# Optimization experiments

Measured on AMD Instinct MI355X. Metric: run time of the kernel, lower is better.

## Reference

```python
import jax, jax.numpy as jnp
import numpy as np

B, S, D, H = 4, 2048, 1024, 16
HD = D // H  # head dim = 64


def setup_inputs() -> dict:
    key = jax.random.key(0)
    ks = jax.random.split(key, 5)
    scale = 0.02
    return {
        "x": jax.random.normal(ks[0], (B, S, D), dtype=jnp.float32),
        "w_qkv": jax.random.normal(ks[1], (D, 3 * D), dtype=jnp.float32) * scale,
        "b_qkv": jax.random.normal(ks[2], (3 * D,), dtype=jnp.float32) * scale,
        "w_proj": jax.random.normal(ks[3], (D, D), dtype=jnp.float32) * scale,
        "b_proj": jax.random.normal(ks[4], (D,), dtype=jnp.float32) * scale,
    }


def reference(x, w_qkv, b_qkv, w_proj, b_proj):
    # Fused QKV projection: [B,S,D] @ [D,3D] -> [B,S,3D]
    qkv = jnp.einsum('bsd,de->bse', x, w_qkv) + b_qkv
    q, k, v = jnp.split(qkv, 3, axis=-1)
    # [B,S,D] -> [B,H,S,hd]
    def heads(t):
        return t.reshape(B, S, H, HD).transpose(0, 2, 1, 3)
    q, k, v = heads(q), heads(k), heads(v)
    # Scaled dot-product attention (non-causal, matching torch SDPA defaults)
    scores = jnp.einsum('bhsd,bhtd->bhst', q, k) / jnp.sqrt(jnp.float32(HD))
    attn = jax.nn.softmax(scores, axis=-1)
    out = jnp.einsum('bhst,bhtd->bhsd', attn, v)
    # [B,H,S,hd] -> [B,S,D]
    out = out.transpose(0, 2, 1, 3).reshape(B, S, D)
    return jnp.einsum('bsd,de->bse', out, w_proj) + b_proj
```

## Files before the change

kernel.cpp:

```cpp
#include <hip/hip_runtime.h>
#include <hip/hip_bf16.h>
#include <cstdint>

typedef __attribute__((ext_vector_type(8))) __bf16 bf16x8;
typedef __attribute__((ext_vector_type(4))) __bf16 bf16x4;
typedef __attribute__((ext_vector_type(4))) float f32x4;

#define MFMA16(a, b, c) __builtin_amdgcn_mfma_f32_16x16x32_bf16(a, b, c, 0, 0, 0)

static constexpr float SCQ = 0.18033688f;

__device__ __forceinline__ void gload16(const void* g, void* l) {
  __builtin_amdgcn_global_load_lds(
      (const __attribute__((address_space(1))) void*)g,
      (__attribute__((address_space(3))) void*)l, 16, 0, 0);
}

__global__ __launch_bounds__(256) void conv_x(const float* __restrict__ in,
                                              __bf16* __restrict__ out) {
  const size_t i = ((size_t)blockIdx.x * 256 + threadIdx.x) * 8;
  const float4 v0 = *(const float4*)(in + i);
  const float4 v1 = *(const float4*)(in + i + 4);
  bf16x8 o = {(__bf16)v0.x, (__bf16)v0.y, (__bf16)v0.z, (__bf16)v0.w,
              (__bf16)v1.x, (__bf16)v1.y, (__bf16)v1.z, (__bf16)v1.w};
  *(bf16x8*)(out + i) = o;
}

__global__ __launch_bounds__(256) void conv_wt(const float* __restrict__ W,
                                               __bf16* __restrict__ Wt,
                                               int K, int N) {
  __shared__ float tile[64][65];
  const int nb = blockIdx.x * 64, kb = blockIdx.y * 64;
  const int t = threadIdx.x, tr = t >> 4, tc = t & 15;
  #pragma unroll
  for (int p = 0; p < 4; ++p) {
    const float4 v =
        *(const float4*)(W + (size_t)(kb + p * 16 + tr) * N + nb + tc * 4);
    tile[p * 16 + tr][tc * 4 + 0] = v.x;
    tile[p * 16 + tr][tc * 4 + 1] = v.y;
    tile[p * 16 + tr][tc * 4 + 2] = v.z;
    tile[p * 16 + tr][tc * 4 + 3] = v.w;
  }
  __syncthreads();
  #pragma unroll
  for (int p = 0; p < 4; ++p) {
    const int n = p * 16 + tr, kk = tc * 4;
    bf16x4 o = {(__bf16)tile[kk + 0][n], (__bf16)tile[kk + 1][n],
                (__bf16)tile[kk + 2][n], (__bf16)tile[kk + 3][n]};
    *(bf16x4*)(Wt + (size_t)(nb + n) * K + kb + kk) = o;
  }
}

__global__ __launch_bounds__(256) void qkv_gemm_b(
    const __bf16* __restrict__ A, const __bf16* __restrict__ Bt,
    const float* __restrict__ bias,
    __bf16* __restrict__ Qb, __bf16* __restrict__ Kb, __bf16* __restrict__ Vt)
{
  __shared__ alignas(16) __bf16 a_sh[128 * 32];
  __shared__ alignas(16) __bf16 b_sh[128 * 32];
  const int id = blockIdx.x;
  const int wg = (id & 7) * 192 + (id >> 3);
  const int n0 = (wg % 24) * 128, m0 = (wg / 24) * 128;
  const int t = threadIdx.x, wave = t >> 6, lane = t & 63;
  const int r = lane & 15, g = lane >> 4;
  const int wm = (wave >> 1) * 64, wn = (wave & 1) * 64;
  f32x4 acc[4][4] = {};

  const int srow = wave * 16 + (lane >> 2);
  const int scol = (lane & 3) * 8;
  const __bf16* gA = A + (size_t)(m0 + srow) * 1024 + scol;
  const __bf16* gB = Bt + (size_t)(n0 + srow) * 1024 + scol;
  __bf16* lA = a_sh + wave * 512;
  __bf16* lB = b_sh + wave * 512;

  for (int k0 = 0; k0 < 1024; k0 += 32) {
    __syncthreads();
    gload16(gA + k0, lA);
    gload16(gA + 64 * 1024 + k0, lA + 2048);
    gload16(gB + k0, lB);
    gload16(gB + 64 * 1024 + k0, lB + 2048);
    __syncthreads();
    bf16x8 af[4], bfr[4];
    #pragma unroll
    for (int i = 0; i < 4; ++i)
      af[i] = *(bf16x8*)&a_sh[(wm + i * 16 + r) * 32 + g * 8];
    #pragma unroll
    for (int j = 0; j < 4; ++j)
      bfr[j] = *(bf16x8*)&b_sh[(wn + j * 16 + r) * 32 + g * 8];
    #pragma unroll
    for (int i = 0; i < 4; ++i)
      #pragma unroll
      for (int j = 0; j < 4; ++j)
        acc[i][j] = MFMA16(af[i], bfr[j], acc[i][j]);
  }

  const int which = n0 >> 10;
  const int bb = m0 >> 11;
  const int sbase = (m0 & 2047) + wm;
  #pragma unroll
  for (int j = 0; j < 4; ++j) {
    const int nc = n0 + wn + j * 16 + r;
    const float bv = bias[nc];
    const int hh = (nc & 1023) >> 6;
    const int d = nc & 63;
    #pragma unroll
    for (int i = 0; i < 4; ++i) {
      const int ss0 = sbase + i * 16 + g * 4;
      if (which == 0) {
        #pragma unroll
        for (int rr = 0; rr < 4; ++rr)
          Qb[((size_t)(bb * 16 + hh) * 2048 + ss0 + rr) * 64 + d] =
              (__bf16)((acc[i][j][rr] + bv) * SCQ);
      } else if (which == 1) {
        #pragma unroll
        for (int rr = 0; rr < 4; ++rr)
          Kb[((size_t)(bb * 16 + hh) * 2048 + ss0 + rr) * 64 + d] =
              (__bf16)(acc[i][j][rr] + bv);
      } else {
        bf16x4 vv;
        #pragma unroll
        for (int rr = 0; rr < 4; ++rr) vv[rr] = (__bf16)(acc[i][j][rr] + bv);
        const int v5 = ss0 & 31;
        const int pcol = (ss0 & ~31) + 8 * ((v5 >> 2) & 3) + 4 * (v5 >> 4);
        *(bf16x4*)&Vt[((size_t)(bb * 16 + hh) * 64 + d) * 2048 + pcol] = vv;
      }
    }
  }
}

__global__ __launch_bounds__(256) void proj_gemm_b(
    const __bf16* __restrict__ A, const __bf16* __restrict__ Bt,
    const float* __restrict__ bias, float* __restrict__ out)
{
  __shared__ alignas(16) __bf16 a_sh[128 * 32];
  __shared__ alignas(16) __bf16 b_sh[128 * 32];
  const int id = blockIdx.x;
  const int wg = (id & 7) * 64 + (id >> 3);
  const int n0 = (wg & 7) * 128, m0 = (wg >> 3) * 128;
  const int t = threadIdx.x, wave = t >> 6, lane = t & 63;
  const int r = lane & 15, g = lane >> 4;
  const int wm = (wave >> 1) * 64, wn = (wave & 1) * 64;
  f32x4 acc[4][4] = {};

  const int srow = wave * 16 + (lane >> 2);
  const int scol = (lane & 3) * 8;
  const __bf16* gA = A + (size_t)(m0 + srow) * 1024 + scol;
  const __bf16* gB = Bt + (size_t)(n0 + srow) * 1024 + scol;
  __bf16* lA = a_sh + wave * 512;
  __bf16* lB = b_sh + wave * 512;

  for (int k0 = 0; k0 < 1024; k0 += 32) {
    __syncthreads();
    gload16(gA + k0, lA);
    gload16(gA + 64 * 1024 + k0, lA + 2048);
    gload16(gB + k0, lB);
    gload16(gB + 64 * 1024 + k0, lB + 2048);
    __syncthreads();
    bf16x8 af[4], bfr[4];
    #pragma unroll
    for (int i = 0; i < 4; ++i)
      af[i] = *(bf16x8*)&a_sh[(wm + i * 16 + r) * 32 + g * 8];
    #pragma unroll
    for (int j = 0; j < 4; ++j)
      bfr[j] = *(bf16x8*)&b_sh[(wn + j * 16 + r) * 32 + g * 8];
    #pragma unroll
    for (int i = 0; i < 4; ++i)
      #pragma unroll
      for (int j = 0; j < 4; ++j)
        acc[i][j] = MFMA16(af[i], bfr[j], acc[i][j]);
  }

  #pragma unroll
  for (int j = 0; j < 4; ++j) {
    const int nc = n0 + wn + j * 16 + r;
    const float bv = bias[nc];
    #pragma unroll
    for (int i = 0; i < 4; ++i)
      #pragma unroll
      for (int rr = 0; rr < 4; ++rr)
        out[(size_t)(m0 + wm + i * 16 + g * 4 + rr) * 1024 + nc] =
            acc[i][j][rr] + bv;
  }
}

__global__ __launch_bounds__(256, 4) void attn_kernel(
    const __bf16* __restrict__ Q, const __bf16* __restrict__ K,
    const __bf16* __restrict__ Vt, __bf16* __restrict__ AO)
{
  __shared__ alignas(16) __bf16 k_sh[64][72];
  __shared__ alignas(16) __bf16 v_sh[64][72];

  const int p = blockIdx.x;
  const int hd = (p & 7) + 8 * (p >> 7);
  const int qt = (p >> 3) & 15;
  const int b = hd >> 4, h = hd & 15;

  const int t = threadIdx.x, wave = t >> 6, lane = t & 63;
  const int r = lane & 15, g = lane >> 4;

  const __bf16* Qp = Q + (size_t)hd * (2048 * 64);
  const __bf16* Kp = K + (size_t)hd * (2048 * 64);
  const __bf16* Vp = Vt + (size_t)hd * (64 * 2048);
  const int q0 = qt * 128 + wave * 32;

  const int sr = t >> 2;
  const int sc = (t & 3) * 8;
  const __bf16* gK = Kp + (size_t)sr * 64 + sc;
  const __bf16* gV = Vp + (size_t)sr * 2048 + sc;

  bf16x8 qf[2][2];
  #pragma unroll
  for (int qh = 0; qh < 2; ++qh)
    #pragma unroll
    for (int hh = 0; hh < 2; ++hh)
      qf[qh][hh] =
          *(const bf16x8*)(Qp + (size_t)(q0 + qh * 16 + r) * 64 + hh * 32 + g * 8);

  float mrun[2] = {0.f, 0.f};
  float lrun[2] = {0.f, 0.f};
  f32x4 o[4][2] = {};

  bf16x8 rk0, rk1, rv0, rv1;
  #define LOADT(kk)                                                \
    {                                                              \
      rk0 = *(const bf16x8*)(gK + (size_t)(kk) * 64);              \
      rk1 = *(const bf16x8*)(gK + (size_t)(kk) * 64 + 32);         \
      rv0 = *(const bf16x8*)(gV + (kk));                           \
      rv1 = *(const bf16x8*)(gV + (kk) + 32);                      \
    }

  LOADT(0);

  for (int t32 = 0; t32 < 32; ++t32) {
    __syncthreads();
    *(bf16x8*)&k_sh[sr][sc] = rk0;
    *(bf16x8*)&k_sh[sr][sc + 32] = rk1;
    *(bf16x8*)&v_sh[sr][sc] = rv0;
    *(bf16x8*)&v_sh[sr][sc + 32] = rv1;
    __syncthreads();
    if (t32 < 31) LOADT((t32 + 1) * 64);

    f32x4 sacc[4][2];
    const f32x4 seed0 = {-mrun[0], -mrun[0], -mrun[0], -mrun[0]};
    const f32x4 seed1 = {-mrun[1], -mrun[1], -mrun[1], -mrun[1]};
    __builtin_amdgcn_s_setprio(1);
    #pragma unroll
    for (int kt = 0; kt < 4; ++kt) {
      const bf16x8 kf0 = *(const bf16x8*)&k_sh[kt * 16 + r][g * 8];
      const bf16x8 kf1 = *(const bf16x8*)&k_sh[kt * 16 + r][32 + g * 8];
      f32x4 s0 = MFMA16(kf0, qf[0][0], seed0);
      s0 = MFMA16(kf1, qf[0][1], s0);
      sacc[kt][0] = s0;
      f32x4 s1 = MFMA16(kf0, qf[1][0], seed1);
      s1 = MFMA16(kf1, qf[1][1], s1);
      sacc[kt][1] = s1;
    }
    __builtin_amdgcn_s_setprio(0);

    bf16x8 pf[2][2];
    #pragma unroll
    for (int qh = 0; qh < 2; ++qh) {
      float a0 = fmaxf(fmaxf(sacc[0][qh][0], sacc[0][qh][1]),
                       fmaxf(sacc[0][qh][2], sacc[0][qh][3]));
      float a1 = fmaxf(fmaxf(sacc[1][qh][0], sacc[1][qh][1]),
                       fmaxf(sacc[1][qh][2], sacc[1][qh][3]));
      float a2 = fmaxf(fmaxf(sacc[2][qh][0], sacc[2][qh][1]),
                       fmaxf(sacc[2][qh][2], sacc[2][qh][3]));
      float a3 = fmaxf(fmaxf(sacc[3][qh][0], sacc[3][qh][1]),
                       fmaxf(sacc[3][qh][2], sacc[3][qh][3]));
      const float tm = fmaxf(fmaxf(a0, a1), fmaxf(a2, a3));

      float s = 0.f;
      if (__any(tm > 6.0f)) {
        float rm = fmaxf(tm, __shfl_xor(tm, 16));
        rm = fmaxf(rm, __shfl_xor(rm, 32));
        const float dl = fmaxf(rm, 0.f);
        const float al = exp2f(-dl);
        mrun[qh] += dl;
        #pragma unroll
        for (int kt = 0; kt < 4; ++kt)
          #pragma unroll
          for (int rr = 0; rr < 4; ++rr) {
            const float e = exp2f(sacc[kt][qh][rr] - dl);
            s += e;
            pf[qh][kt >> 1][(kt & 1) * 4 + rr] = (__bf16)e;
          }
        lrun[qh] = lrun[qh] * al + s;
        #pragma unroll
        for (int dt = 0; dt < 4; ++dt)
          #pragma unroll
          for (int rr = 0; rr < 4; ++rr)
            o[dt][qh][rr] *= al;
      } else {
        #pragma unroll
        for (int kt = 0; kt < 4; ++kt)
          #pragma unroll
          for (int rr = 0; rr < 4; ++rr) {
            const float e = exp2f(sacc[kt][qh][rr]);
            s += e;
            pf[qh][kt >> 1][(kt & 1) * 4 + rr] = (__bf16)e;
          }
        lrun[qh] += s;
      }
    }

    __builtin_amdgcn_s_setprio(1);
    #pragma unroll
    for (int c = 0; c < 2; ++c)
      #pragma unroll
      for (int dt = 0; dt < 4; ++dt) {
        const bf16x8 vf = *(const bf16x8*)&v_sh[dt * 16 + r][c * 32 + g * 8];
        o[dt][0] = MFMA16(vf, pf[0][c], o[dt][0]);
        o[dt][1] = MFMA16(vf, pf[1][c], o[dt][1]);
      }
    __builtin_amdgcn_s_setprio(0);
  }
  #undef LOADT

  #pragma unroll
  for (int qh = 0; qh < 2; ++qh) {
    float lr = lrun[qh];
    lr += __shfl_xor(lr, 16);
    lr += __shfl_xor(lr, 32);
    const float inv = 1.0f / lr;
    const int ss = q0 + qh * 16 + r;
    #pragma unroll
    for (int dt = 0; dt < 4; ++dt) {
      bf16x4 ov;
      #pragma unroll
      for (int rr = 0; rr < 4; ++rr)
        ov[rr] = (__bf16)(o[dt][qh][rr] * inv);
      *(bf16x4*)&AO[((size_t)b * 2048 + ss) * 1024 + h * 64 + dt * 16 + 4 * g] = ov;
    }
  }
}

extern "C" void kernel_launch(void* const* d_in, const int* in_sizes, int n_in,
                              void* d_out, int out_size, void* d_ws, size_t ws_size,
                              hipStream_t stream) {
  (void)in_sizes; (void)n_in; (void)out_size; (void)ws_size;
  const float* x      = (const float*)d_in[0];
  const float* w_qkv  = (const float*)d_in[1];
  const float* b_qkv  = (const float*)d_in[2];
  const float* w_proj = (const float*)d_in[3];
  const float* b_proj = (const float*)d_in[4];
  float* out = (float*)d_out;

  char* ws = (char*)d_ws;
  const size_t E2 = (size_t)8192 * 1024 * 2;
  __bf16* Qb  = (__bf16*)(ws);
  __bf16* Kb  = (__bf16*)(ws + E2);
  __bf16* Vt  = (__bf16*)(ws + 2 * E2);
  __bf16* Xb  = (__bf16*)(ws + 3 * E2);
  __bf16* AO  = Xb;
  __bf16* Wqt = (__bf16*)(ws + 4 * E2);
  __bf16* Wpt = (__bf16*)(ws + 4 * E2 + (size_t)3072 * 1024 * 2);

  conv_x<<<4096, 256, 0, stream>>>(x, Xb);
  conv_wt<<<dim3(48, 16), 256, 0, stream>>>(w_qkv, Wqt, 1024, 3072);
  conv_wt<<<dim3(16, 16), 256, 0, stream>>>(w_proj, Wpt, 1024, 1024);
  qkv_gemm_b<<<1536, 256, 0, stream>>>(Xb, Wqt, b_qkv, Qb, Kb, Vt);
  attn_kernel<<<1024, 256, 0, stream>>>(Qb, Kb, Vt, AO);
  proj_gemm_b<<<512, 256, 0, stream>>>(AO, Wpt, b_proj, out);
}
```

Before: 244.9 us.

## Double-buffer attention K/V tiles via direct global-to-LDS loads with XOR swizzle

The attention kernel now stages K and V tiles straight into LDS with global_load_lds into two ping-pong buffers, replacing the register-staged copy that needed two barriers per iteration. The QKV GEMM writes K and V in a pre-swizzled layout (XOR on 16-byte chunks by row) so the unpadded 128-byte rows read without bank conflicts. The intent is to overlap the next tile's load with compute, drop the register round trip, and cut to one barrier per iteration. In exchange LDS use grows to 32KB per block, which may limit occupancy at 4 blocks per CU, and the layout change couples the two kernels.

```diff
diff --git a/kernel.cpp b/kernel.cpp
--- a/kernel.cpp
+++ b/kernel.cpp
@@ -114,7 +114,8 @@
       } else if (which == 1) {
         #pragma unroll
         for (int rr = 0; rr < 4; ++rr)
-          Kb[((size_t)(bb * 16 + hh) * 2048 + ss0 + rr) * 64 + d] =
+          Kb[((size_t)(bb * 16 + hh) * 2048 + ss0 + rr) * 64 +
+             (d ^ ((((ss0 + rr) & 7)) << 3))] =
               (__bf16)(acc[i][j][rr] + bv);
       } else {
         bf16x4 vv;
@@ -122,7 +123,8 @@
         for (int rr = 0; rr < 4; ++rr) vv[rr] = (__bf16)(acc[i][j][rr] + bv);
         const int v5 = ss0 & 31;
         const int pcol = (ss0 & ~31) + 8 * ((v5 >> 2) & 3) + 4 * (v5 >> 4);
-        *(bf16x4*)&Vt[((size_t)(bb * 16 + hh) * 64 + d) * 2048 + pcol] = vv;
+        const int scol2 = (pcol & ~127) | ((pcol & 127) ^ ((d & 7) << 3));
+        *(bf16x4*)&Vt[((size_t)(bb * 16 + hh) * 64 + d) * 2048 + scol2] = vv;
       }
     }
   }
@@ -187,8 +189,7 @@
     const __bf16* __restrict__ Q, const __bf16* __restrict__ K,
     const __bf16* __restrict__ Vt, __bf16* __restrict__ AO)
 {
-  __shared__ alignas(16) __bf16 k_sh[64][72];
-  __shared__ alignas(16) __bf16 v_sh[64][72];
+  __shared__ alignas(16) char lds[2][16384];
 
   const int p = blockIdx.x;
   const int hd = (p & 7) + 8 * (p >> 7);
@@ -199,14 +200,9 @@
   const int r = lane & 15, g = lane >> 4;
 
   const __bf16* Qp = Q + (size_t)hd * (2048 * 64);
-  const __bf16* Kp = K + (size_t)hd * (2048 * 64);
-  const __bf16* Vp = Vt + (size_t)hd * (64 * 2048);
+  const char* Kh = (const char*)(K + (size_t)hd * (2048 * 64));
+  const char* Vh = (const char*)(Vt + (size_t)hd * (64 * 2048));
   const int q0 = qt * 128 + wave * 32;
-
-  const int sr = t >> 2;
-  const int sc = (t & 3) * 8;
-  const __bf16* gK = Kp + (size_t)sr * 64 + sc;
-  const __bf16* gV = Vp + (size_t)sr * 2048 + sc;
 
   bf16x8 qf[2][2];
   #pragma unroll
@@ -220,25 +216,33 @@
   float lrun[2] = {0.f, 0.f};
   f32x4 o[4][2] = {};
 
-  bf16x8 rk0, rk1, rv0, rv1;
-  #define LOADT(kk)                                                \
-    {                                                              \
-      rk0 = *(const bf16x8*)(gK + (size_t)(kk) * 64);              \
-      rk1 = *(const bf16x8*)(gK + (size_t)(kk) * 64 + 32);         \
-      rv0 = *(const bf16x8*)(gV + (kk));                           \
-      rv1 = *(const bf16x8*)(gV + (kk) + 32);                      \
-    }
-
-  LOADT(0);
+  const int lofs0 = wave * 1024;
+  const int gofs0 = wave * 1024 + lane * 16;
+
+  #define STAGE(t32, bi)                                                  \
+    {                                                                     \
+      char* lb = lds[bi];                                                 \
+      _Pragma("unroll")                                                   \
+      for (int rnd = 0; rnd < 2; ++rnd) {                                 \
+        const int fb = rnd * 4096 + gofs0;                                \
+        gload16(Kh + (size_t)(t32) * 8192 + fb, lb + rnd * 4096 + lofs0); \
+        gload16(Vh + (size_t)(fb >> 7) * 4096 + (size_t)(t32) * 128 +     \
+                    (fb & 127),                                           \
+                lb + 8192 + rnd * 4096 + lofs0);                          \
+      }                                                                   \
+    }
+
+  STAGE(0, 0);
+  __syncthreads();
+
+  const int sw = (r & 7) << 4;
 
   for (int t32 = 0; t32 < 32; ++t32) {
-    __syncthreads();
-    *(bf16x8*)&k_sh[sr][sc] = rk0;
-    *(bf16x8*)&k_sh[sr][sc + 32] = rk1;
-    *(bf16x8*)&v_sh[sr][sc] = rv0;
-    *(bf16x8*)&v_sh[sr][sc + 32] = rv1;
-    __syncthreads();
-    if (t32 < 31) LOADT((t32 + 1) * 64);
+    const int cur = t32 & 1;
+    if (t32 < 31) STAGE(t32 + 1, cur ^ 1);
+
+    const char* kb = lds[cur];
+    const char* vb = lds[cur] + 8192;
 
     f32x4 sacc[4][2];
     const f32x4 seed0 = {-mrun[0], -mrun[0], -mrun[0], -mrun[0]};
@@ -246,8 +250,9 @@
     __builtin_amdgcn_s_setprio(1);
     #pragma unroll
     for (int kt = 0; kt < 4; ++kt) {
-      const bf16x8 kf0 = *(const bf16x8*)&k_sh[kt * 16 + r][g * 8];
-      const bf16x8 kf1 = *(const bf16x8*)&k_sh[kt * 16 + r][32 + g * 8];
+      const int rowb = (kt * 16 + r) * 128;
+      const bf16x8 kf0 = *(const bf16x8*)(kb + rowb + ((16 * g) ^ sw));
+      const bf16x8 kf1 = *(const bf16x8*)(kb + rowb + ((64 + 16 * g) ^ sw));
       f32x4 s0 = MFMA16(kf0, qf[0][0], seed0);
       s0 = MFMA16(kf1, qf[0][1], s0);
       sacc[kt][0] = s0;
@@ -309,13 +314,16 @@
     for (int c = 0; c < 2; ++c)
       #pragma unroll
       for (int dt = 0; dt < 4; ++dt) {
-        const bf16x8 vf = *(const bf16x8*)&v_sh[dt * 16 + r][c * 32 + g * 8];
+        const bf16x8 vf = *(const bf16x8*)(vb + (dt * 16 + r) * 128 +
+                                           ((c * 64 + 16 * g) ^ sw));
         o[dt][0] = MFMA16(vf, pf[0][c], o[dt][0]);
         o[dt][1] = MFMA16(vf, pf[1][c], o[dt][1]);
       }
     __builtin_amdgcn_s_setprio(0);
-  }
-  #undef LOADT
+
+    __syncthreads();
+  }
+  #undef STAGE
 
   #pragma unroll
   for (int qh = 0; qh < 2; ++qh) {
```

Measured after the change: 245.6 us. About the same (+0.3%).
